# Kernel optimization log

Measured on AMD Instinct MI355X. Metric: run time of the kernel, lower is better.

The kernel has to match this reference:

```python
import jax, jax.numpy as jnp
import numpy as np

# Static config (from init_kwargs)
IMAGE_RES_OUT = 64
IMAGE_UPSCALE = 2
FREQ_RES_OUT = 16
FREQ_UPSCALE = 4
IMAGE_RES = IMAGE_RES_OUT * IMAGE_UPSCALE      # 128 internal spatial res
FREQ_RES = FREQ_RES_OUT * FREQ_UPSCALE          # 64 internal velocity channels
CUBE_FOV_HALF = 1000.0                          # pc
F_REST_CO21 = 230.538                           # GHz, CO(2-1) rest frequency
C_KMS = 299792.458                              # speed of light km/s


def setup_inputs() -> dict:
    half_bw = F_REST_CO21 * 400.0 / C_KMS  # frequency half-bandwidth ~ +-400 km/s
    freqs = jnp.linspace(F_REST_CO21 - half_bw, F_REST_CO21 + half_bw,
                         FREQ_RES_OUT, dtype=jnp.float32)
    f32 = lambda v: jnp.asarray(v, jnp.float32)
    return {
        "freqs": freqs,
        "inclination": f32(0.8),        # rad
        "sky_rot": f32(0.5),            # rad
        "line_broadening": f32(30.0),   # km/s
        "velocity_shift": f32(10.0),    # km/s
        "v_max": f32(250.0),            # km/s  (velocity model param)
        "r_turn": f32(150.0),           # pc    (velocity model param)
        "i0": f32(1.0),                 # intensity model amplitude
        "r_d": f32(300.0),              # pc    disk scale length
        "h_z": f32(50.0),               # pc    disk scale height
    }


def _rot_matrix(inclination, sky_rot, dtype):
    ci, si = jnp.cos(inclination), jnp.sin(inclination)
    cr, sr = jnp.cos(sky_rot), jnp.sin(sky_rot)
    zero = jnp.zeros((), dtype)
    one = jnp.ones((), dtype)
    Rz = jnp.stack([jnp.stack([cr, -sr, zero]),
                    jnp.stack([sr, cr, zero]),
                    jnp.stack([zero, zero, one])])
    Rx = jnp.stack([jnp.stack([one, zero, zero]),
                    jnp.stack([zero, ci, -si]),
                    jnp.stack([zero, si, ci])])
    return Rx @ Rz  # DoRotation; DoRotationT uses its transpose


def reference(freqs, inclination, sky_rot, line_broadening, velocity_shift,
              v_max, r_turn, i0, r_d, h_z):
    dtype = freqs.dtype
    # 3D simulation meshgrid [X, Y, Z], side IMAGE_RES
    lin = jnp.linspace(-CUBE_FOV_HALF, CUBE_FOV_HALF, IMAGE_RES, dtype=dtype)
    x, y, z = jnp.meshgrid(lin, lin, lin, indexing='ij')

    R = _rot_matrix(inclination, sky_rot, dtype)
    coords = jnp.stack([x, y, z], axis=-1)                 # [X,Y,Z,3]
    rc = jnp.einsum('ab,xyzb->axyz', R, coords)            # DoRotation
    rx, ry, rz = rc[0], rc[1], rc[2]

    # velocity model: arctan rotation curve in galaxy plane
    rad = jnp.sqrt(rx * rx + ry * ry + jnp.asarray(1e-12, dtype))
    v_abs = v_max * (2.0 / jnp.pi) * jnp.arctan(rad / r_turn)
    v_abs = jnp.nan_to_num(v_abs, posinf=0.0, neginf=0.0)

    theta = jnp.arctan2(ry, rx)
    v_x = -v_abs * jnp.sin(theta)
    v_y = v_abs * jnp.cos(theta)
    # DoRotationT: inverse rotation of velocity vector (v_z input is 0);
    # only the line-of-sight (z) component is used downstream.
    RT = R.T
    v_los = RT[2, 0] * v_x + RT[2, 1] * v_y                # [X,Y,Z]

    # intensity model: exponential disk
    intensity = i0 * jnp.exp(-rad / r_d) * jnp.exp(-jnp.abs(rz) / h_z)  # [X,Y,Z]

    # upsampled frequency axis -> velocity labels (systemic, CO21)
    df = (freqs[-1] - freqs[0]) / (FREQ_RES - 1)
    freqs_up = freqs[0] + df * (jnp.arange(FREQ_RES, dtype=dtype)
                                - 0.5 * FREQ_UPSCALE)       # [F]
    vel_labels = C_KMS * (F_REST_CO21 - freqs_up) / F_REST_CO21  # [F] km/s

    sig_sq = line_broadening ** 2
    # Gaussian-KDE soft binning: [X,Y,F,Z] kernel reduced over Z
    diff = vel_labels[None, None, :, None] - (v_los[:, :, None, :] + velocity_shift)
    kde = jnp.exp(-(diff * diff) / sig_sq)
    cube = jnp.einsum('xyfz,xyz->xyf', kde, intensity)
    cube = cube * (1.0 / jnp.sqrt(2.0 * jnp.pi * sig_sq))   # [X,Y,F]

    # permute to (F, X, Y) and avg_pool3d (FREQ_UPSCALE, IMAGE_UPSCALE, IMAGE_UPSCALE)
    cube3d = jnp.transpose(cube, (2, 0, 1))
    c = cube3d.reshape(FREQ_RES_OUT, FREQ_UPSCALE,
                       IMAGE_RES_OUT, IMAGE_UPSCALE,
                       IMAGE_RES_OUT, IMAGE_UPSCALE)
    return c.mean(axis=(1, 3, 5))                           # [16, 64, 64]
```

## Files before the change

### kernel.cpp

```cpp
#include <hip/hip_runtime.h>
#include <math.h>

#define IMG_OUT 64
#define WIN 14
#define PSTRIDE 17

__global__ __launch_bounds__(64) void cube_sim_kernel(
    const float* __restrict__ freqs,
    const float* __restrict__ p_incl,
    const float* __restrict__ p_rot,
    const float* __restrict__ p_lb,
    const float* __restrict__ p_vshift,
    const float* __restrict__ p_vmax,
    const float* __restrict__ p_rturn,
    const float* __restrict__ p_i0,
    const float* __restrict__ p_rd,
    const float* __restrict__ p_hz,
    float* __restrict__ out)
{
    const int lane = threadIdx.x;
    const int xo = blockIdx.x, yo = blockIdx.y;
    const int p  = lane >> 4;
    const int zb = lane & 15;

    __shared__ float s_P[64 * PSTRIDE + 4];

    const float incl   = p_incl[0];
    const float rot    = p_rot[0];
    const float lb     = p_lb[0];
    const float vshift = p_vshift[0];
    const float vmx    = p_vmax[0];
    const float rturn  = p_rturn[0];
    const float i0     = p_i0[0];
    const float rd     = p_rd[0];
    const float hz     = p_hz[0];

    const float LOG2E = 1.4426950408889634f;
    const float ci = __cosf(incl), si = __sinf(incl);
    const float cr = __cosf(rot),  sr = __sinf(rot);

    const float K1   = 299792.458f / 230.538f;
    const float f_lo = freqs[0];
    const float df   = (freqs[15] - f_lo) * (1.0f / 63.0f);
    const float beta = K1 * df;
    const float alpha = 299792.458f - K1 * (f_lo - 2.0f * df) - vshift;
    const float inv_beta = __builtin_amdgcn_rcpf(beta);

    const float rlb = __builtin_amdgcn_rcpf(lb);
    const float sgs = 1.20112240878645f * rlb;
    const float bp  = beta * sgs;

    const float step  = 2000.0f / 127.0f;
    const float invrt = __builtin_amdgcn_rcpf(rturn);
    const float cA_r  = -LOG2E * __builtin_amdgcn_rcpf(rd);
    const float cA_z  = -LOG2E * __builtin_amdgcn_rcpf(hz);

    const float x = -1000.0f + (float)(2 * xo + (p >> 1)) * step;
    const float y = -1000.0f + (float)(2 * yo + (p & 1)) * step;
    const float rx   = cr * x - sr * y;
    const float u0   = sr * x + cr * y;
    const float crx  = -si * vmx * 0.636619772367581f * rx;
    const float rx2e = fmaf(rx, rx, 1e-12f);
    const float zb0  = -1000.0f + (float)(zb * 8) * step;

    float v[8], A[8];
    #pragma unroll
    for (int k = 0; k < 8; ++k) {
        const float z  = zb0 + (float)k * step;
        const float ry = ci * u0 - si * z;
        const float rz = si * u0 + ci * z;
        const float r2 = fmaf(ry, ry, rx2e);
        const float ir = __builtin_amdgcn_rsqf(r2);
        const float rad = r2 * ir;
        const float tg = rad * invrt;
        const float tm = fminf(tg, __builtin_amdgcn_rcpf(tg));
        const float x2 = tm * tm;
        float pl = fmaf(x2, 0.0208351f, -0.0851330f);
        pl = fmaf(x2, pl, 0.1801410f);
        pl = fmaf(x2, pl, -0.3302995f);
        pl = fmaf(x2, pl, 0.9998660f);
        pl *= tm;
        const float at = (tg > 1.0f) ? (1.57079632679f - pl) : pl;
        v[k] = crx * at * ir;
        A[k] = fmaf(rad, cA_r, fabsf(rz) * cA_z);
    }

    float vlo = v[0], vhi = v[0];
    #pragma unroll
    for (int k = 1; k < 8; ++k) { vlo = fminf(vlo, v[k]); vhi = fmaxf(vhi, v[k]); }
    const float mid = 0.5f * (vlo + vhi);
    int basei = (int)floorf((alpha - mid) * inv_beta) - 6;
    basei = min(max(basei, 0), 64 - WIN);
    const float Wb = fmaf(-beta, (float)basei, alpha);

    float acc[WIN];
    #pragma unroll
    for (int j = 0; j < WIN; ++j) acc[j] = 0.0f;

    #pragma unroll
    for (int k = 0; k < 8; ++k) {
        const float Wk = sgs * (Wb - v[k]);
        const float Ak = A[k];
        #pragma unroll
        for (int j = 0; j < WIN; ++j) {
            const float d = fmaf(-bp, (float)j, Wk);
            acc[j] += __builtin_amdgcn_exp2f(fmaf(-d, d, Ak));
        }
    }

    const int rowb = lane * PSTRIDE;
    float P = 0.0f;
    s_P[rowb] = 0.0f;
    #pragma unroll
    for (int j = 0; j < WIN; ++j) { P += acc[j]; s_P[rowb + j + 1] = P; }
    __syncthreads();

    const int t16 = lane & 15;
    const int g   = lane >> 4;
    const int c4  = t16 * 4;
    float s = 0.0f;
    #pragma unroll
    for (int i = 0; i < 16; ++i) {
        const int r = g * 16 + i;
        const int b = __shfl(basei, r);
        int lo = c4 - b;
        int hi = lo + 4;
        lo = min(max(lo, 0), WIN);
        hi = min(max(hi, 0), WIN);
        s += s_P[r * PSTRIDE + hi] - s_P[r * PSTRIDE + lo];
    }
    s += __shfl_xor(s, 16);
    s += __shfl_xor(s, 32);

    if (lane < 16) {
        const float scale = i0 * 0.0625f * 0.3989422804014327f * rlb;
        out[t16 * (IMG_OUT * IMG_OUT) + xo * IMG_OUT + yo] = s * scale;
    }
}

extern "C" void kernel_launch(void* const* d_in, const int* in_sizes, int n_in,
                              void* d_out, int out_size, void* d_ws, size_t ws_size,
                              hipStream_t stream) {
    (void)in_sizes; (void)n_in; (void)d_ws; (void)ws_size; (void)out_size;
    const float* freqs  = (const float*)d_in[0];
    const float* incl   = (const float*)d_in[1];
    const float* rot    = (const float*)d_in[2];
    const float* lb     = (const float*)d_in[3];
    const float* vshift = (const float*)d_in[4];
    const float* vmax   = (const float*)d_in[5];
    const float* rturn  = (const float*)d_in[6];
    const float* i0     = (const float*)d_in[7];
    const float* rd     = (const float*)d_in[8];
    const float* hz     = (const float*)d_in[9];
    float* out = (float*)d_out;

    dim3 grid(IMG_OUT, IMG_OUT);
    dim3 block(64);
    hipLaunchKernelGGL(cube_sim_kernel, grid, block, 0, stream,
                       freqs, incl, rot, lb, vshift, vmax, rturn, i0, rd, hz, out);
}
```

Before: 13.23 us.

## Split z-range across two waves per block and shrink velocity window

```diff
diff --git a/kernel.cpp b/kernel.cpp
--- a/kernel.cpp
+++ b/kernel.cpp
@@ -2,10 +2,10 @@
 #include <math.h>
 
 #define IMG_OUT 64
-#define WIN 14
-#define PSTRIDE 17
+#define WIN 12
+#define PSTRIDE 13
 
-__global__ __launch_bounds__(64) void cube_sim_kernel(
+__global__ __launch_bounds__(128, 8) void cube_sim_kernel(
     const float* __restrict__ freqs,
     const float* __restrict__ p_incl,
     const float* __restrict__ p_rot,
@@ -18,12 +18,16 @@
     const float* __restrict__ p_hz,
     float* __restrict__ out)
 {
-    const int lane = threadIdx.x;
+    const int t    = threadIdx.x;
+    const int w    = t >> 6;
+    const int lane = t & 63;
+    const int p    = lane >> 4;
+    const int zseg = (w << 4) | (lane & 15);
     const int xo = blockIdx.x, yo = blockIdx.y;
-    const int p  = lane >> 4;
-    const int zb = lane & 15;
 
-    __shared__ float s_P[64 * PSTRIDE + 4];
+    __shared__ float s_P[128 * PSTRIDE];
+    __shared__ int   s_base[128];
+    __shared__ float s_part[2][16];
 
     const float incl   = p_incl[0];
     const float rot    = p_rot[0];
@@ -61,12 +65,12 @@
     const float u0   = sr * x + cr * y;
     const float crx  = -si * vmx * 0.636619772367581f * rx;
     const float rx2e = fmaf(rx, rx, 1e-12f);
-    const float zb0  = -1000.0f + (float)(zb * 8) * step;
+    const float z0   = -1000.0f + (float)(zseg * 4) * step;
 
-    float v[8], A[8];
+    float v[4], A[4];
     #pragma unroll
-    for (int k = 0; k < 8; ++k) {
-        const float z  = zb0 + (float)k * step;
+    for (int k = 0; k < 4; ++k) {
+        const float z  = z0 + (float)k * step;
         const float ry = ci * u0 - si * z;
         const float rz = si * u0 + ci * z;
         const float r2 = fmaf(ry, ry, rx2e);
@@ -85,11 +89,10 @@
         A[k] = fmaf(rad, cA_r, fabsf(rz) * cA_z);
     }
 
-    float vlo = v[0], vhi = v[0];
-    #pragma unroll
-    for (int k = 1; k < 8; ++k) { vlo = fminf(vlo, v[k]); vhi = fmaxf(vhi, v[k]); }
+    float vlo = fminf(fminf(v[0], v[1]), fminf(v[2], v[3]));
+    float vhi = fmaxf(fmaxf(v[0], v[1]), fmaxf(v[2], v[3]));
     const float mid = 0.5f * (vlo + vhi);
-    int basei = (int)floorf((alpha - mid) * inv_beta) - 6;
+    int basei = (int)floorf((alpha - mid) * inv_beta) - 5;
     basei = min(max(basei, 0), 64 - WIN);
     const float Wb = fmaf(-beta, (float)basei, alpha);
 
@@ -98,7 +101,7 @@
     for (int j = 0; j < WIN; ++j) acc[j] = 0.0f;
 
     #pragma unroll
-    for (int k = 0; k < 8; ++k) {
+    for (int k = 0; k < 4; ++k) {
         const float Wk = sgs * (Wb - v[k]);
         const float Ak = A[k];
         #pragma unroll
@@ -108,21 +111,22 @@
         }
     }
 
-    const int rowb = lane * PSTRIDE;
+    const int rowb = t * PSTRIDE;
     float P = 0.0f;
     s_P[rowb] = 0.0f;
     #pragma unroll
     for (int j = 0; j < WIN; ++j) { P += acc[j]; s_P[rowb + j + 1] = P; }
+    s_base[t] = basei;
     __syncthreads();
 
-    const int t16 = lane & 15;
-    const int g   = lane >> 4;
-    const int c4  = t16 * 4;
+    const int c  = t & 15;
+    const int g  = t >> 4;
+    const int c4 = c * 4;
     float s = 0.0f;
     #pragma unroll
     for (int i = 0; i < 16; ++i) {
         const int r = g * 16 + i;
-        const int b = __shfl(basei, r);
+        const int b = s_base[r];
         int lo = c4 - b;
         int hi = lo + 4;
         lo = min(max(lo, 0), WIN);
@@ -131,10 +135,13 @@
     }
     s += __shfl_xor(s, 16);
     s += __shfl_xor(s, 32);
+    if (lane < 16) s_part[w][lane] = s;
+    __syncthreads();
 
-    if (lane < 16) {
+    if (t < 16) {
+        const float sum = s_part[0][t] + s_part[1][t];
         const float scale = i0 * 0.0625f * 0.3989422804014327f * rlb;
-        out[t16 * (IMG_OUT * IMG_OUT) + xo * IMG_OUT + yo] = s * scale;
+        out[t * (IMG_OUT * IMG_OUT) + xo * IMG_OUT + yo] = sum * scale;
     }
 }
 
@@ -155,7 +162,7 @@
     float* out = (float*)d_out;
 
     dim3 grid(IMG_OUT, IMG_OUT);
-    dim3 block(64);
+    dim3 block(128);
     hipLaunchKernelGGL(cube_sim_kernel, grid, block, 0, stream,
                        freqs, incl, rot, lb, vshift, vmax, rturn, i0, rd, hz, out);
 }
```

Result: slower. 14.39 us (+8.8%).
